# Kernel optimization log

Hardware: AMD Instinct MI355X
Metric: run time of the kernel (lower is better)

Reference implementation:

```python
import jax, jax.numpy as jnp
import numpy as np

N, M, E, B = 50000, 4, 400000, 64
NHID, EMBED, NOUT, NLAYER = 64, 64, 1, 3


def _glorot(k, shape):
    fan_in = shape[0]
    return jax.random.normal(k, shape, jnp.float32) / np.float32(np.sqrt(fan_in))


def setup_inputs() -> dict:
    key = jax.random.key(0)
    ks = jax.random.split(key, 18)
    inp = {
        "additional_x": jax.random.normal(ks[0], (N, M, 1), jnp.float32),
        "edge_index": jax.random.randint(ks[1], (2, E), 0, N, dtype=jnp.int32),
        "batch": jnp.sort(jax.random.randint(ks[2], (N,), 0, B, dtype=jnp.int32)),
        # conv layer 0: in_channels=1, layers 1,2: in_channels=NHID (bias=False since bn='BN')
        "Wself0": _glorot(ks[3], (1, NHID)),
        "Wnei0": _glorot(ks[4], (1, NHID)),
        "Wself1": _glorot(ks[5], (NHID, NHID)),
        "Wnei1": _glorot(ks[6], (NHID, NHID)),
        "Wself2": _glorot(ks[7], (NHID, NHID)),
        "Wnei2": _glorot(ks[8], (NHID, NHID)),
        # inter_encoder: MLP(nlayer*nhid -> nhid -> nhid -> EMBED), no norm, relu between
        "W1": _glorot(ks[9], (NLAYER * NHID, NHID)),
        "b1": jnp.zeros((NHID,), jnp.float32),
        "W2": _glorot(ks[10], (NHID, NHID)),
        "b2": jnp.zeros((NHID,), jnp.float32),
        "W3": _glorot(ks[11], (NHID, EMBED)),
        "b3": jnp.zeros((EMBED,), jnp.float32),
        # output_encoder: single Linear (with_final_activation=False)
        "Wo": _glorot(ks[12], (EMBED, NOUT)),
        "bo": jnp.zeros((NOUT,), jnp.float32),
    }
    return inp


def reference(additional_x, edge_index, batch,
              Wself0, Wnei0, Wself1, Wnei1, Wself2, Wnei2,
              W1, b1, W2, b2, W3, b3, Wo, bo):
    src, dst = edge_index[0], edge_index[1]

    def conv(x, Ws, Wn):
        # GraphConv: W_self x_i + W_neigh * sum_{j in N(i)} x_j   (x: [N, M, Din])
        agg = jax.ops.segment_sum(x[src], dst, num_segments=N)  # [N, M, Din]
        return jnp.einsum('nmd,dh->nmh', x, Ws) + jnp.einsum('nmd,dh->nmh', agg, Wn)

    x = additional_x  # [N, M, 1]
    skips = []
    for Ws, Wn in ((Wself0, Wnei0), (Wself1, Wnei1), (Wself2, Wnei2)):
        x = jax.nn.relu(conv(x, Ws, Wn))  # [N, M, NHID]
        skips.append(x)
    x = jnp.concatenate(skips, axis=-1)  # [N, M, NLAYER*NHID]

    # inter_encoder (3-layer MLP, no norm)
    h = jax.nn.relu(x @ W1 + b1)
    h = jax.nn.relu(h @ W2 + b2)
    h = h @ W3 + b3  # [N, M, EMBED]

    g = h.mean(axis=-2)  # [N, EMBED]
    g = 2.0 * (g - g.min()) / (g.max() - g.min())

    # pooling == 'add': scatter-add over graphs
    pooled = jax.ops.segment_sum(g, batch, num_segments=B)  # [B, EMBED]

    # output_encoder: plain linear
    return pooled @ Wo + bo  # [B, NOUT]
```

## Files before the change

### kernel.cpp

```cpp
#include <hip/hip_runtime.h>
#include <math.h>

#define NN 50000
#define MM 4
#define EE 400000
#define BB 64
#define NROWS (NN*MM)
#define NBLK_SCAN 98

typedef __attribute__((ext_vector_type(8))) short bf16x8;
typedef __attribute__((ext_vector_type(4))) float f32x4;

struct f8 { float4 lo, hi; };


__device__ __forceinline__ unsigned enc_f(float f) {
  unsigned u = __float_as_uint(f);
  return (u & 0x80000000u) ? ~u : (u | 0x80000000u);
}
__device__ __forceinline__ float dec_f(unsigned u) {
  return (u & 0x80000000u) ? __uint_as_float(u ^ 0x80000000u) : __uint_as_float(~u);
}

__device__ __forceinline__ unsigned short bf16rn(float f) {
  unsigned u = __float_as_uint(f);
  return (unsigned short)((u + 0x7FFFu + ((u >> 16) & 1u)) >> 16);
}
__device__ __forceinline__ float bf2f(unsigned short h) {
  return __uint_as_float(((unsigned)h) << 16);
}

__device__ __forceinline__ int swzc(int row, int col) {
  return ((((col >> 3) ^ (row & 7)) << 3)) | (col & 7);
}

__device__ __forceinline__ f8 zero8() {
  f8 r; r.lo = make_float4(0.f,0.f,0.f,0.f); r.hi = r.lo; return r;
}
__device__ __forceinline__ void add8(f8& a, const f8& b) {
  a.lo.x += b.lo.x; a.lo.y += b.lo.y; a.lo.z += b.lo.z; a.lo.w += b.lo.w;
  a.hi.x += b.hi.x; a.hi.y += b.hi.y; a.hi.z += b.hi.z; a.hi.w += b.hi.w;
}
__device__ __forceinline__ f8 b2f8(bf16x8 v) {
  f8 r;
  r.lo = make_float4(bf2f((unsigned short)v[0]), bf2f((unsigned short)v[1]),
                     bf2f((unsigned short)v[2]), bf2f((unsigned short)v[3]));
  r.hi = make_float4(bf2f((unsigned short)v[4]), bf2f((unsigned short)v[5]),
                     bf2f((unsigned short)v[6]), bf2f((unsigned short)v[7]));
  return r;
}
__device__ __forceinline__ bf16x8 f2b8(const f8& v) {
  bf16x8 h;
  h[0] = (short)bf16rn(v.lo.x); h[1] = (short)bf16rn(v.lo.y);
  h[2] = (short)bf16rn(v.lo.z); h[3] = (short)bf16rn(v.lo.w);
  h[4] = (short)bf16rn(v.hi.x); h[5] = (short)bf16rn(v.hi.y);
  h[6] = (short)bf16rn(v.hi.z); h[7] = (short)bf16rn(v.hi.w);
  return h;
}
__device__ __forceinline__ f8 conv0f8(float xv, float av, const f8& ws, const f8& wn) {
  f8 t;
  t.lo.x = fmaxf(fmaf(xv, ws.lo.x, av * wn.lo.x), 0.f);
  t.lo.y = fmaxf(fmaf(xv, ws.lo.y, av * wn.lo.y), 0.f);
  t.lo.z = fmaxf(fmaf(xv, ws.lo.z, av * wn.lo.z), 0.f);
  t.lo.w = fmaxf(fmaf(xv, ws.lo.w, av * wn.lo.w), 0.f);
  t.hi.x = fmaxf(fmaf(xv, ws.hi.x, av * wn.hi.x), 0.f);
  t.hi.y = fmaxf(fmaf(xv, ws.hi.y, av * wn.hi.y), 0.f);
  t.hi.z = fmaxf(fmaf(xv, ws.hi.z, av * wn.hi.z), 0.f);
  t.hi.w = fmaxf(fmaf(xv, ws.hi.w, av * wn.hi.w), 0.f);
  return t;
}


__global__ void hist_k(const int* __restrict__ ei, int* __restrict__ deg) {
  int e = blockIdx.x * blockDim.x + threadIdx.x;
  if (e < EE) atomicAdd(&deg[ei[EE + e]], 1);
}

__global__ __launch_bounds__(512) void scan1_k(const int* __restrict__ deg,
                                               int* __restrict__ rowstart,
                                               int* __restrict__ bsum) {
  __shared__ int s[512];
  int i = blockIdx.x * 512 + threadIdx.x;
  int v = (i < NN) ? deg[i] : 0;
  s[threadIdx.x] = v;
  __syncthreads();
  for (int off = 1; off < 512; off <<= 1) {
    int t = (threadIdx.x >= (unsigned)off) ? s[threadIdx.x - off] : 0;
    __syncthreads();
    s[threadIdx.x] += t;
    __syncthreads();
  }
  if (i < NN) rowstart[i] = s[threadIdx.x] - v;
  if (threadIdx.x == 511) bsum[blockIdx.x] = s[511];
}

__global__ void scan2_k(int* __restrict__ bsum) {
  if (threadIdx.x == 0) {
    int acc = 0;
    for (int k = 0; k < NBLK_SCAN; ++k) { int t = bsum[k]; bsum[k] = acc; acc += t; }
  }
}

__global__ __launch_bounds__(512) void scan3_k(int* __restrict__ rowstart,
                                               int* __restrict__ cursor,
                                               const int* __restrict__ bsum) {
  int i = blockIdx.x * 512 + threadIdx.x;
  if (i < NN) {
    int v = rowstart[i] + bsum[blockIdx.x];
    rowstart[i] = v;
    cursor[i] = v;
  }
  if (i == 0) rowstart[NN] = EE;
}

__global__ void fill_k(const int* __restrict__ ei, int* __restrict__ cursor,
                       int* __restrict__ nbr) {
  int e = blockIdx.x * blockDim.x + threadIdx.x;
  if (e >= EE) return;
  int d = ei[EE + e];
  int p = atomicAdd(&cursor[d], 1);
  nbr[p] = ei[e];
}


__global__ void prepw_k(const float* __restrict__ Ws1, const float* __restrict__ Wn1,
                        const float* __restrict__ Ws2, const float* __restrict__ Wn2,
                        const float* __restrict__ W1,  const float* __restrict__ W2,
                        const float* __restrict__ W3,  unsigned short* __restrict__ wt) {
  int idx = blockIdx.x * 256 + threadIdx.x;
  if (idx >= 9 * 4096) return;
  int m = idx >> 12, r = idx & 4095;
  int c = r >> 6, k = r & 63;
  const float* src = Ws1;
  switch (m) {
    case 0: src = Ws1; break;
    case 1: src = Wn1; break;
    case 2: src = Ws2; break;
    case 3: src = W1 + 64 * 64; break;
    case 4: src = Wn2; break;
    case 5: src = W1 + 128 * 64; break;
    case 6: src = W1; break;
    case 7: src = W2; break;
    case 8: src = W3; break;
  }
  wt[idx] = bf16rn(src[k * 64 + c]);
}


__global__ void agg0_gather_k(const float* __restrict__ x0,
                              const int* __restrict__ rowstart,
                              const int* __restrict__ nbr,
                              float* __restrict__ agg0) {
  int idx = blockIdx.x * blockDim.x + threadIdx.x;
  if (idx >= NROWS) return;
  int n = idx >> 2, m = idx & 3;
  int beg = rowstart[n], end = rowstart[n + 1];
  float acc = 0.0f;
  for (int i = beg; i < end; ++i) acc += x0[nbr[i] * 4 + m];
  agg0[idx] = acc;
}


#define STAGE_WT(mi)                                                        \
  *(bf16x8*)&WTl[tid >> 3][(((tid & 7) ^ ((tid >> 3) & 7)) << 3)] =         \
      ((const bf16x8*)((const short*)wt + (mi) * 4096))[tid];

#define MFMA_PHASE(A0, A1)                                                   \
  _Pragma("unroll")                                                          \
  for (int kh = 0; kh < 2; ++kh) {                                           \
    int aslot = (kh << 2) | (lane >> 4);                                     \
    int scol  = ((aslot ^ (fl & 7)) << 3);                                   \
    bf16x8 af  = *(const bf16x8*)&XAs[mrow0 + fl][scol];                     \
    bf16x8 bf0 = *(const bf16x8*)&WTl[ncol0 + fl][scol];                     \
    bf16x8 bf1 = *(const bf16x8*)&WTl[ncol0 + 16 + fl][scol];                \
    A0 = __builtin_amdgcn_mfma_f32_16x16x32_bf16(af, bf0, A0, 0, 0, 0);      \
    A1 = __builtin_amdgcn_mfma_f32_16x16x32_bf16(af, bf1, A1, 0, 0, 0);      \
  }

#define DCOMMIT_RELU(A0, A1)                                            \
  _Pragma("unroll")                                                     \
  for (int j = 0; j < 4; ++j) {                                         \
    XAs[drow + j][swzc(drow + j, dc0)] = bf16rn(fmaxf(A0[j], 0.f));     \
    XAs[drow + j][swzc(drow + j, dc1)] = bf16rn(fmaxf(A1[j], 0.f));     \
  }

#define XSLOT(rr, cc8) ((((cc8) >> 3) ^ ((rr) & 7)) << 3)


__global__ __launch_bounds__(512, 4) void conv1_k(const float* __restrict__ x0,
                                                  const float* __restrict__ agg0,
                                                  const int* __restrict__ rowstart,
                                                  const int* __restrict__ nbr,
                                                  const float* __restrict__ Ws0,
                                                  const float* __restrict__ Wn0,
                                                  const unsigned short* __restrict__ wt,
                                                  unsigned short* __restrict__ x1b) {
  __shared__ unsigned short XAs[64][64];
  __shared__ unsigned short WTl[64][64];
  const int row0 = blockIdx.x << 6;
  const int nb0  = blockIdx.x << 4;
  const int tid = threadIdx.x;
  const int r   = tid >> 3;
  const int c8  = (tid & 7) << 3;
  const int lane  = tid & 63;
  const int wid   = tid >> 6;
  const int mrow0 = (wid >> 1) << 4;
  const int ncol0 = (wid & 1) << 5;
  const int fl    = lane & 15;
  const int drow  = mrow0 + ((lane >> 4) << 2);
  const int dc0   = ncol0 + fl, dc1 = ncol0 + 16 + fl;

  const int n = nb0 + (r >> 2), m = r & 3;
  const int beg = rowstart[n], end = rowstart[n + 1];

  f8 ws8, wn8;
  ws8.lo = *(const float4*)(Ws0 + c8); ws8.hi = *(const float4*)(Ws0 + c8 + 4);
  wn8.lo = *(const float4*)(Wn0 + c8); wn8.hi = *(const float4*)(Wn0 + c8 + 4);

  *(bf16x8*)&XAs[r][XSLOT(r, c8)] =
      f2b8(conv0f8(x0[row0 + r], agg0[row0 + r], ws8, wn8));
  STAGE_WT(0);

  f8 ga;
  {
    f8 a0 = zero8(), a1 = zero8();
    int i = beg;
    for (; i + 4 <= end; i += 4) {
      int s0 = nbr[i] * 4 + m, s1 = nbr[i+1] * 4 + m;
      int s2 = nbr[i+2] * 4 + m, s3 = nbr[i+3] * 4 + m;
      float xv0 = x0[s0], av0 = agg0[s0];
      float xv1 = x0[s1], av1 = agg0[s1];
      float xv2 = x0[s2], av2 = agg0[s2];
      float xv3 = x0[s3], av3 = agg0[s3];
      f8 t0 = conv0f8(xv0, av0, ws8, wn8); add8(a0, t0);
      f8 t1 = conv0f8(xv1, av1, ws8, wn8); add8(a1, t1);
      f8 t2 = conv0f8(xv2, av2, ws8, wn8); add8(a0, t2);
      f8 t3 = conv0f8(xv3, av3, ws8, wn8); add8(a1, t3);
    }
    bool p0 = i < end, p1 = i + 1 < end, p2 = i + 2 < end;
    float xv0 = 0.f, av0 = 0.f, xv1 = 0.f, av1 = 0.f, xv2 = 0.f, av2 = 0.f;
    if (p0) { int s = nbr[i]     * 4 + m; xv0 = x0[s]; av0 = agg0[s]; }
    if (p1) { int s = nbr[i + 1] * 4 + m; xv1 = x0[s]; av1 = agg0[s]; }
    if (p2) { int s = nbr[i + 2] * 4 + m; xv2 = x0[s]; av2 = agg0[s]; }
    if (p0) { f8 t = conv0f8(xv0, av0, ws8, wn8); add8(a0, t); }
    if (p1) { f8 t = conv0f8(xv1, av1, ws8, wn8); add8(a1, t); }
    if (p2) { f8 t = conv0f8(xv2, av2, ws8, wn8); add8(a0, t); }
    add8(a0, a1);
    ga = a0;
  }
  __syncthreads();

  f32x4 a0v = {0.f,0.f,0.f,0.f}, a1v = {0.f,0.f,0.f,0.f};
  MFMA_PHASE(a0v, a1v);
  __syncthreads();
  *(bf16x8*)&XAs[r][XSLOT(r, c8)] = f2b8(ga);
  STAGE_WT(1);
  __syncthreads();

  MFMA_PHASE(a0v, a1v);
  __syncthreads();
  DCOMMIT_RELU(a0v, a1v);
  __syncthreads();

  *(bf16x8*)(x1b + (size_t)(row0 + r) * 64 + c8) =
      *(const bf16x8*)&XAs[r][XSLOT(r, c8)];
}


__global__ __launch_bounds__(512, 4) void fused2_k(const unsigned short* __restrict__ x1b,
    const int* __restrict__ rowstart, const int* __restrict__ nbr,
    const float* __restrict__ x0, const float* __restrict__ agg0,
    const float* __restrict__ Ws0, const float* __restrict__ Wn0,
    const unsigned short* __restrict__ wt,
    const float* __restrict__ b1, const float* __restrict__ b2,
    const float* __restrict__ b3,
    float* __restrict__ g, unsigned* __restrict__ mm) {
  __shared__ unsigned short XAs[64][64];
  __shared__ unsigned short WTl[64][64];
  __shared__ float red[16];
  const int row0 = blockIdx.x << 6;
  const int nb0  = blockIdx.x << 4;
  const int tid = threadIdx.x;
  const int r   = tid >> 3;
  const int c8  = (tid & 7) << 3;
  const int lane  = tid & 63;
  const int wid   = tid >> 6;
  const int mrow0 = (wid >> 1) << 4;
  const int ncol0 = (wid & 1) << 5;
  const int fl    = lane & 15;
  const int drow  = mrow0 + ((lane >> 4) << 2);
  const int dc0   = ncol0 + fl, dc1 = ncol0 + 16 + fl;

  const int n = nb0 + (r >> 2), m = r & 3;
  const int beg = rowstart[n], end = rowstart[n + 1];

  *(bf16x8*)&XAs[r][XSLOT(r, c8)] =
      *(const bf16x8*)(x1b + (size_t)(row0 + r) * 64 + c8);
  STAGE_WT(2);

  f8 ga;
  {
    f8 a0 = zero8(), a1 = zero8();
    int i = beg;
    for (; i + 4 <= end; i += 4) {
      bf16x8 v0 = *(const bf16x8*)(x1b + (size_t)(nbr[i]   * 4 + m) * 64 + c8);
      bf16x8 v1 = *(const bf16x8*)(x1b + (size_t)(nbr[i+1] * 4 + m) * 64 + c8);
      bf16x8 v2 = *(const bf16x8*)(x1b + (size_t)(nbr[i+2] * 4 + m) * 64 + c8);
      bf16x8 v3 = *(const bf16x8*)(x1b + (size_t)(nbr[i+3] * 4 + m) * 64 + c8);
      f8 t0 = b2f8(v0); add8(a0, t0);
      f8 t1 = b2f8(v1); add8(a1, t1);
      f8 t2 = b2f8(v2); add8(a0, t2);
      f8 t3 = b2f8(v3); add8(a1, t3);
    }
    bool q0 = i < end, q1 = i + 1 < end, q2 = i + 2 < end;
    bf16x8 v0 = {}, v1 = {}, v2 = {};
    if (q0) v0 = *(const bf16x8*)(x1b + (size_t)(nbr[i]     * 4 + m) * 64 + c8);
    if (q1) v1 = *(const bf16x8*)(x1b + (size_t)(nbr[i + 1] * 4 + m) * 64 + c8);
    if (q2) v2 = *(const bf16x8*)(x1b + (size_t)(nbr[i + 2] * 4 + m) * 64 + c8);
    if (q0) { f8 t = b2f8(v0); add8(a0, t); }
    if (q1) { f8 t = b2f8(v1); add8(a1, t); }
    if (q2) { f8 t = b2f8(v2); add8(a0, t); }
    add8(a0, a1);
    ga = a0;
  }
  __syncthreads();

  f32x4 accP0 = {0.f,0.f,0.f,0.f}, accP1 = {0.f,0.f,0.f,0.f};
  MFMA_PHASE(accP0, accP1);
  __syncthreads();
  STAGE_WT(3);
  __syncthreads();

  f32x4 accQ0, accQ1;
  {
    float bv0 = b1[dc0], bv1 = b1[dc1];
    accQ0[0]=bv0; accQ0[1]=bv0; accQ0[2]=bv0; accQ0[3]=bv0;
    accQ1[0]=bv1; accQ1[1]=bv1; accQ1[2]=bv1; accQ1[3]=bv1;
  }
  MFMA_PHASE(accQ0, accQ1);
  __syncthreads();
  *(bf16x8*)&XAs[r][XSLOT(r, c8)] = f2b8(ga);
  STAGE_WT(4);
  __syncthreads();

  MFMA_PHASE(accP0, accP1);
  __syncthreads();
  DCOMMIT_RELU(accP0, accP1);
  STAGE_WT(5);
  __syncthreads();

  MFMA_PHASE(accQ0, accQ1);
  __syncthreads();
  {
    f8 ws8, wn8;
    ws8.lo = *(const float4*)(Ws0 + c8); ws8.hi = *(const float4*)(Ws0 + c8 + 4);
    wn8.lo = *(const float4*)(Wn0 + c8); wn8.hi = *(const float4*)(Wn0 + c8 + 4);
    *(bf16x8*)&XAs[r][XSLOT(r, c8)] =
        f2b8(conv0f8(x0[row0 + r], agg0[row0 + r], ws8, wn8));
  }
  STAGE_WT(6);
  __syncthreads();

  MFMA_PHASE(accQ0, accQ1);
  __syncthreads();
  DCOMMIT_RELU(accQ0, accQ1);
  STAGE_WT(7);
  __syncthreads();

  f32x4 accR0, accR1;
  {
    float bv0 = b2[dc0], bv1 = b2[dc1];
    accR0[0]=bv0; accR0[1]=bv0; accR0[2]=bv0; accR0[3]=bv0;
    accR1[0]=bv1; accR1[1]=bv1; accR1[2]=bv1; accR1[3]=bv1;
  }
  MFMA_PHASE(accR0, accR1);
  __syncthreads();
  DCOMMIT_RELU(accR0, accR1);
  STAGE_WT(8);
  __syncthreads();

  f32x4 accS0, accS1;
  {
    float bv0 = b3[dc0], bv1 = b3[dc1];
    accS0[0]=bv0; accS0[1]=bv0; accS0[2]=bv0; accS0[3]=bv0;
    accS1[0]=bv1; accS1[1]=bv1; accS1[2]=bv1; accS1[3]=bv1;
  }
  MFMA_PHASE(accS0, accS1);
  __syncthreads();
#pragma unroll
  for (int j = 0; j < 4; ++j) {
    XAs[drow + j][swzc(drow + j, dc0)] = bf16rn(accS0[j]);
    XAs[drow + j][swzc(drow + j, dc1)] = bf16rn(accS1[j]);
  }
  __syncthreads();

  float lmin = 3.4e38f, lmax = -3.4e38f;
  for (int k = tid; k < 1024; k += 512) {
    int nl = k >> 6, c = k & 63;
    float s = 0.25f * (bf2f(XAs[4*nl+0][swzc(4*nl+0, c)]) +
                       bf2f(XAs[4*nl+1][swzc(4*nl+1, c)]) +
                       bf2f(XAs[4*nl+2][swzc(4*nl+2, c)]) +
                       bf2f(XAs[4*nl+3][swzc(4*nl+3, c)]));
    g[(size_t)((row0 >> 2) + nl) * 64 + c] = s;
    lmin = fminf(lmin, s);
    lmax = fmaxf(lmax, s);
  }
#pragma unroll
  for (int off = 32; off; off >>= 1) {
    lmin = fminf(lmin, __shfl_xor(lmin, off));
    lmax = fmaxf(lmax, __shfl_xor(lmax, off));
  }
  if ((tid & 63) == 0) { red[tid >> 6] = lmin; red[8 + (tid >> 6)] = lmax; }
  __syncthreads();
  if (tid == 0) {
    float m0 = red[0], m1 = red[8];
#pragma unroll
    for (int w = 1; w < 8; ++w) {
      m0 = fminf(m0, red[w]);
      m1 = fmaxf(m1, red[8 + w]);
    }
    atomicMin(&mm[0], enc_f(m0));
    atomicMax(&mm[1], enc_f(m1));
  }
}


__global__ __launch_bounds__(256) void pool2_k(const float* __restrict__ g,
                                               const int* __restrict__ batch,
                                               const unsigned* __restrict__ mm,
                                               float* __restrict__ pooled) {
  int c = threadIdx.x & 63;
  int grp = threadIdx.x >> 6;
  int base = blockIdx.x * 64 + grp * 16;
  float gmin = dec_f(mm[0]);
  float sc = 2.0f / (dec_f(mm[1]) - gmin);
  float acc = 0.0f; int cur = -1;
  for (int i = 0; i < 16; ++i) {
    int n = base + i;
    if (n >= NN) break;
    int b = batch[n];
    if (b != cur) {
      if (cur >= 0) unsafeAtomicAdd(&pooled[(cur << 6) + c], acc);
      cur = b; acc = 0.0f;
    }
    acc += (g[(size_t)n * 64 + c] - gmin) * sc;
  }
  if (cur >= 0) unsafeAtomicAdd(&pooled[(cur << 6) + c], acc);
}


__global__ void out_k(const float* __restrict__ pooled, const float* __restrict__ Wo,
                      const float* __restrict__ bo, float* __restrict__ out) {
  int b = blockIdx.x, l = threadIdx.x;
  float v = pooled[(b << 6) + l] * Wo[l];
#pragma unroll
  for (int off = 32; off; off >>= 1) v += __shfl_xor(v, off);
  if (l == 0) out[b] = v + bo[0];
}


extern "C" void kernel_launch(void* const* d_in, const int* in_sizes, int n_in,
                              void* d_out, int out_size, void* d_ws, size_t ws_size,
                              hipStream_t stream) {
  const float* x0   = (const float*)d_in[0];
  const int*   ei   = (const int*)d_in[1];
  const int*   batch= (const int*)d_in[2];
  const float* Ws0  = (const float*)d_in[3];
  const float* Wn0  = (const float*)d_in[4];
  const float* Ws1  = (const float*)d_in[5];
  const float* Wn1  = (const float*)d_in[6];
  const float* Ws2  = (const float*)d_in[7];
  const float* Wn2  = (const float*)d_in[8];
  const float* W1   = (const float*)d_in[9];
  const float* b1   = (const float*)d_in[10];
  const float* W2   = (const float*)d_in[11];
  const float* b2   = (const float*)d_in[12];
  const float* W3   = (const float*)d_in[13];
  const float* b3   = (const float*)d_in[14];
  const float* Wo   = (const float*)d_in[15];
  const float* bo   = (const float*)d_in[16];
  float* out = (float*)d_out;

  unsigned short* x1b = (unsigned short*)d_ws;
  unsigned short* wt  = x1b + (size_t)NROWS * 64;
  float* agg0   = (float*)(wt + 9 * 4096);
  float* g      = agg0 + NROWS;
  float* pooled = g    + (size_t)NN * 64;
  unsigned* mm  = (unsigned*)(pooled + BB * 64);
  int* deg      = (int*)(mm + 2);
  int* rowstart = deg + NN;
  int* cursor   = rowstart + NN + 1;
  int* nbr      = cursor + NN;
  int* bsum     = nbr + EE;

  hipMemsetAsync(deg, 0, NN * sizeof(int), stream);
  hist_k<<<(EE + 255) / 256, 256, 0, stream>>>(ei, deg);
  prepw_k<<<144, 256, 0, stream>>>(Ws1, Wn1, Ws2, Wn2, W1, W2, W3, wt);
  scan1_k<<<NBLK_SCAN, 512, 0, stream>>>(deg, rowstart, bsum);
  scan2_k<<<1, 64, 0, stream>>>(bsum);
  scan3_k<<<NBLK_SCAN, 512, 0, stream>>>(rowstart, cursor, bsum);
  fill_k<<<(EE + 255) / 256, 256, 0, stream>>>(ei, cursor, nbr);

  agg0_gather_k<<<(NROWS + 255) / 256, 256, 0, stream>>>(x0, rowstart, nbr, agg0);

  conv1_k<<<NROWS / 64, 512, 0, stream>>>(x0, agg0, rowstart, nbr,
                                          Ws0, Wn0, wt, x1b);

  hipMemsetAsync(mm, 0xFF, 4, stream);
  hipMemsetAsync(mm + 1, 0x00, 4, stream);
  fused2_k<<<NROWS / 64, 512, 0, stream>>>(x1b, rowstart, nbr, x0, agg0,
                                           Ws0, Wn0, wt, b1, b2, b3, g, mm);

  hipMemsetAsync(pooled, 0, BB * 64 * sizeof(float), stream);
  pool2_k<<<(NN + 63) / 64, 256, 0, stream>>>(g, batch, mm, pooled);

  out_k<<<BB, 64, 0, stream>>>(pooled, Wo, bo, out);
}
```

Baseline: 210.8 us.

## Fuse pooling and output linear into one segment-per-block kernel, drop memsets

Replaces the atomic scatter-add pooling kernel and the separate output kernel with one kernel per graph. Each block binary-searches the sorted batch array for its segment bounds, then computes a dot product of the rescaled g with Wo, applying the min-max scale after the reduction. The min/max sentinel initialisation moves into the weight-prep kernel, which removes three memset launches and the pooled buffer. Only 64 blocks stream all of g, so memory parallelism may be lower than in the 782-block atomic version.

```diff
diff --git a/kernel.cpp b/kernel.cpp
--- a/kernel.cpp
+++ b/kernel.cpp
@@ -126,8 +126,10 @@
 __global__ void prepw_k(const float* __restrict__ Ws1, const float* __restrict__ Wn1,
                         const float* __restrict__ Ws2, const float* __restrict__ Wn2,
                         const float* __restrict__ W1,  const float* __restrict__ W2,
-                        const float* __restrict__ W3,  unsigned short* __restrict__ wt) {
+                        const float* __restrict__ W3,  unsigned short* __restrict__ wt,
+                        unsigned* __restrict__ mm) {
   int idx = blockIdx.x * 256 + threadIdx.x;
+  if (idx == 0) { mm[0] = 0xFFFFFFFFu; mm[1] = 0u; }
   if (idx >= 9 * 4096) return;
   int m = idx >> 12, r = idx & 4095;
   int c = r >> 6, k = r & 63;
@@ -425,37 +427,40 @@
 }
 
 
-__global__ __launch_bounds__(256) void pool2_k(const float* __restrict__ g,
-                                               const int* __restrict__ batch,
-                                               const unsigned* __restrict__ mm,
-                                               float* __restrict__ pooled) {
-  int c = threadIdx.x & 63;
-  int grp = threadIdx.x >> 6;
-  int base = blockIdx.x * 64 + grp * 16;
-  float gmin = dec_f(mm[0]);
-  float sc = 2.0f / (dec_f(mm[1]) - gmin);
-  float acc = 0.0f; int cur = -1;
-  for (int i = 0; i < 16; ++i) {
-    int n = base + i;
-    if (n >= NN) break;
-    int b = batch[n];
-    if (b != cur) {
-      if (cur >= 0) unsafeAtomicAdd(&pooled[(cur << 6) + c], acc);
-      cur = b; acc = 0.0f;
+__global__ __launch_bounds__(256) void poolout_k(const float* __restrict__ g,
+                                                 const int* __restrict__ batch,
+                                                 const unsigned* __restrict__ mm,
+                                                 const float* __restrict__ Wo,
+                                                 const float* __restrict__ bo,
+                                                 float* __restrict__ out) {
+  __shared__ int seg[2];
+  __shared__ float red[4];
+  const int b = blockIdx.x;
+  const int tid = threadIdx.x;
+  if (tid < 2) {
+    int target = b + tid;
+    int lo = 0, hi = NN;
+    while (lo < hi) {
+      int mid = (lo + hi) >> 1;
+      if (batch[mid] < target) lo = mid + 1; else hi = mid;
     }
-    acc += (g[(size_t)n * 64 + c] - gmin) * sc;
-  }
-  if (cur >= 0) unsafeAtomicAdd(&pooled[(cur << 6) + c], acc);
-}
-
-
-__global__ void out_k(const float* __restrict__ pooled, const float* __restrict__ Wo,
-                      const float* __restrict__ bo, float* __restrict__ out) {
-  int b = blockIdx.x, l = threadIdx.x;
-  float v = pooled[(b << 6) + l] * Wo[l];
+    seg[tid] = lo;
+  }
+  __syncthreads();
+  const int lo = seg[0], hi = seg[1];
+  const float gmin = dec_f(mm[0]);
+  const float sc = 2.0f / (dec_f(mm[1]) - gmin);
+  const int c = tid & 63;
+  const float wv = Wo[c];
+  float acc = 0.f;
+  for (int nn = lo + (tid >> 6); nn < hi; nn += 4)
+    acc += (g[(size_t)nn * 64 + c] - gmin) * wv;
 #pragma unroll
-  for (int off = 32; off; off >>= 1) v += __shfl_xor(v, off);
-  if (l == 0) out[b] = v + bo[0];
+  for (int off = 32; off; off >>= 1) acc += __shfl_xor(acc, off);
+  if ((tid & 63) == 0) red[tid >> 6] = acc;
+  __syncthreads();
+  if (tid == 0)
+    out[b] = sc * (red[0] + red[1] + red[2] + red[3]) + bo[0];
 }
 
 
@@ -485,8 +490,7 @@
   unsigned short* wt  = x1b + (size_t)NROWS * 64;
   float* agg0   = (float*)(wt + 9 * 4096);
   float* g      = agg0 + NROWS;
-  float* pooled = g    + (size_t)NN * 64;
-  unsigned* mm  = (unsigned*)(pooled + BB * 64);
+  unsigned* mm  = (unsigned*)(g + (size_t)NN * 64);
   int* deg      = (int*)(mm + 2);
   int* rowstart = deg + NN;
   int* cursor   = rowstart + NN + 1;
@@ -495,7 +499,7 @@
 
   hipMemsetAsync(deg, 0, NN * sizeof(int), stream);
   hist_k<<<(EE + 255) / 256, 256, 0, stream>>>(ei, deg);
-  prepw_k<<<144, 256, 0, stream>>>(Ws1, Wn1, Ws2, Wn2, W1, W2, W3, wt);
+  prepw_k<<<144, 256, 0, stream>>>(Ws1, Wn1, Ws2, Wn2, W1, W2, W3, wt, mm);
   scan1_k<<<NBLK_SCAN, 512, 0, stream>>>(deg, rowstart, bsum);
   scan2_k<<<1, 64, 0, stream>>>(bsum);
   scan3_k<<<NBLK_SCAN, 512, 0, stream>>>(rowstart, cursor, bsum);
@@ -506,13 +510,8 @@
   conv1_k<<<NROWS / 64, 512, 0, stream>>>(x0, agg0, rowstart, nbr,
                                           Ws0, Wn0, wt, x1b);
 
-  hipMemsetAsync(mm, 0xFF, 4, stream);
-  hipMemsetAsync(mm + 1, 0x00, 4, stream);
   fused2_k<<<NROWS / 64, 512, 0, stream>>>(x1b, rowstart, nbr, x0, agg0,
                                            Ws0, Wn0, wt, b1, b2, b3, g, mm);
 
-  hipMemsetAsync(pooled, 0, BB * 64 * sizeof(float), stream);
-  pool2_k<<<(NN + 63) / 64, 256, 0, stream>>>(g, batch, mm, pooled);
-
-  out_k<<<BB, 64, 0, stream>>>(pooled, Wo, bo, out);
-}
+  poolout_k<<<BB, 256, 0, stream>>>(g, batch, mm, Wo, bo, out);
+}
```

After: 246.7 us. 1.17x slower.
